# Performance work log

Measured on AMD Instinct MI355X. Metric: run time of the kernel, lower is better.

## Reference

```python
import jax, jax.numpy as jnp
import numpy as np

NEG_SLOPE = 0.2  # PyG GATConv default leaky_relu slope


def gat_conv(x, src, dst, W, a_src, a_dst, b, num_nodes):
    """One PyG-style GATConv layer (concat over heads).
    x: [N, F_in]; src/dst: [E] (message flows src -> dst);
    W: [F_in, H*C]; a_src/a_dst: [H, C]; b: [H*C].
    """
    H, C = a_src.shape
    h = (x @ W).reshape(num_nodes, H, C)              # [N, H, C]
    alpha_src = jnp.sum(h * a_src, axis=-1)           # [N, H]
    alpha_dst = jnp.sum(h * a_dst, axis=-1)           # [N, H]
    e = jax.nn.leaky_relu(alpha_src[src] + alpha_dst[dst], NEG_SLOPE)  # [E, H]
    # segment softmax over incoming edges of each destination node
    m = jax.ops.segment_max(e, dst, num_segments=num_nodes)            # [N, H]
    ex = jnp.exp(e - m[dst])
    s = jax.ops.segment_sum(ex, dst, num_segments=num_nodes)           # [N, H]
    alpha = ex / (s[dst] + 1e-16)                                      # [E, H]
    msg = h[src] * alpha[:, :, None]                                   # [E, H, C]
    out = jax.ops.segment_sum(msg, dst, num_segments=num_nodes)        # [N, H, C]
    return out.reshape(num_nodes, H * C) + b


def setup_inputs() -> dict:
    key = jax.random.key(0)
    ks = jax.random.split(key, 12)
    N, E, F_in, C, H = 50000, 800000, 256, 64, 8
    x = jax.random.normal(ks[0], (N, F_in), dtype=jnp.float32)
    edge_index = jax.random.randint(ks[1], (2, E), 0, N, dtype=jnp.int64)
    glorot = lambda k, shape: jax.random.normal(k, shape, jnp.float32) * np.sqrt(2.0 / (shape[0] + shape[-1]))
    return {
        "x": x,
        "edge_index": edge_index,
        "W1": glorot(ks[2], (F_in, H * C)),
        "att_src1": glorot(ks[3], (H, C)),
        "att_dst1": glorot(ks[4], (H, C)),
        "b1": jnp.zeros((H * C,), jnp.float32),
        "W2": glorot(ks[5], (H * C, 1 * C)),
        "att_src2": glorot(ks[6], (1, C)),
        "att_dst2": glorot(ks[7], (1, C)),
        "b2": jnp.zeros((C,), jnp.float32),
    }


def reference(x, edge_index, W1, att_src1, att_dst1, b1, W2, att_src2, att_dst2, b2):
    N = x.shape[0]
    # add self-loops (PyG GATConv default add_self_loops=True)
    loops = jnp.arange(N, dtype=edge_index.dtype)
    src = jnp.concatenate([edge_index[0], loops])
    dst = jnp.concatenate([edge_index[1], loops])
    h = gat_conv(x, src, dst, W1, att_src1, att_dst1, b1, N)   # [N, 512]
    h = jax.nn.relu(h)                                         # dropout p=0 -> identity
    out = gat_conv(h, src, dst, W2, att_src2, att_dst2, b2, N) # [N, 64]
    return out
```

## Files before the change

kernel.cpp:

```cpp
#include <hip/hip_runtime.h>
#include <hip/hip_bf16.h>
#include <math.h>
#include <type_traits>

#define NEG_SLOPE 0.2f
#define CAP 64

typedef float f32x4 __attribute__((ext_vector_type(4)));
typedef short s16x8 __attribute__((ext_vector_type(8)));
typedef short s16x4 __attribute__((ext_vector_type(4)));

__device__ __forceinline__ float bf2f(ushort s) {
    union { unsigned u; float f; } cv; cv.u = ((unsigned)s) << 16;
    return cv.f;
}
__device__ __forceinline__ ushort f2bf(float f) {
    __hip_bfloat16 b = __float2bfloat16(f);
    union { __hip_bfloat16 b; ushort u; } cv; cv.b = b;
    return cv.u;
}

__device__ __forceinline__ int edge_val(const int* e, long long i, int is64) {
    return is64 ? e[(size_t)(2 * i)] : e[(size_t)i];
}

__global__ __launch_bounds__(256) void prep_k(
        const float* __restrict__ W1, ushort* __restrict__ W1t, int K1, int N1,
        const float* __restrict__ W2, ushort* __restrict__ W2t, int K2, int N2,
        int* __restrict__ counts, int N, int nbW1, int nbW2) {
    int b = blockIdx.x, tid = threadIdx.x;
    if (b < nbW1) {
        int idx = b * 256 + tid;
        if (idx < K1 * N1) {
            int k = idx & (K1 - 1), n = idx / K1;
            W1t[(size_t)n * K1 + k] = f2bf(W1[(size_t)k * N1 + n]);
        }
        return;
    }
    b -= nbW1;
    if (b < nbW2) {
        int idx = b * 256 + tid;
        if (idx < K2 * N2) {
            int k = idx & (K2 - 1), n = idx / K2;
            W2t[(size_t)n * K2 + k] = f2bf(W2[(size_t)k * N2 + n]);
        }
        return;
    }
    b -= nbW2;
    int i = b * 256 + tid;
    if (i < N) counts[i] = 0;
}

template <typename AT, int KK, int NCOLS, int H, int HB>
__device__ __forceinline__ void gemm_bres_core(
        int bx, int by, const AT* __restrict__ A, const ushort* __restrict__ Bt,
        ushort* __restrict__ C,
        const float* __restrict__ att_s, const float* __restrict__ att_d,
        float* __restrict__ as_, float* __restrict__ ad_, int M, int Ntot) {
    constexpr int NT = NCOLS / 16;
    __shared__ __align__(16) ushort Bs[NCOLS][KK + 8];

    int tid = threadIdx.x;
    int wid = tid >> 6, lane = tid & 63;
    int l15 = lane & 15, l4 = lane >> 4;
    int bn = bx * NCOLS;

#pragma unroll
    for (int p = 0; p < NCOLS * KK / (8 * 512); ++p) {
        int idx = p * 512 + tid;
        int n = idx / (KK / 8);
        int kc = (idx % (KK / 8)) << 3;
        *(s16x8*)&Bs[n][kc] = *(const s16x8*)&Bt[(size_t)(bn + n) * KK + kc];
    }

    int mbase = by * 128 + wid * 16;
    int rowA = mbase + l15; if (rowA >= M) rowA = M - 1;
    s16x8 af[KK / 32];
    if constexpr (std::is_same_v<AT, float>) {
        const float* Ap = A + (size_t)rowA * KK + (l4 << 3);
#pragma unroll
        for (int ks = 0; ks < KK / 32; ++ks) {
            float4 u0 = *(const float4*)&Ap[ks * 32];
            float4 u1 = *(const float4*)&Ap[ks * 32 + 4];
            s16x8 w;
            w[0] = (short)f2bf(u0.x); w[1] = (short)f2bf(u0.y);
            w[2] = (short)f2bf(u0.z); w[3] = (short)f2bf(u0.w);
            w[4] = (short)f2bf(u1.x); w[5] = (short)f2bf(u1.y);
            w[6] = (short)f2bf(u1.z); w[7] = (short)f2bf(u1.w);
            af[ks] = w;
        }
    } else {
        const ushort* Ap = A + (size_t)rowA * KK + (l4 << 3);
#pragma unroll
        for (int ks = 0; ks < KK / 32; ++ks) af[ks] = *(const s16x8*)&Ap[ks * 32];
    }

    __syncthreads();

    f32x4 acc[NT] = {};
#pragma unroll
    for (int nt = 0; nt < NT; ++nt) {
#pragma unroll
        for (int ks = 0; ks < KK / 32; ++ks) {
            s16x8 bfr = *(const s16x8*)&Bs[nt * 16 + l15][ks * 32 + (l4 << 3)];
            acc[nt] = __builtin_amdgcn_mfma_f32_16x16x32_bf16(af[ks], bfr, acc[nt], 0, 0, 0);
        }
    }

#pragma unroll
    for (int h = 0; h < HB; ++h) {
        int head = bx * HB + h;
        float asv[4], adv[4];
#pragma unroll
        for (int t = 0; t < 4; ++t) {
            asv[t] = att_s[head * 64 + t * 16 + l15];
            adv[t] = att_d[head * 64 + t * 16 + l15];
        }
#pragma unroll
        for (int j = 0; j < 4; ++j) {
            int r = mbase + (l4 << 2) + j;
            float ps = 0.f, pd = 0.f;
#pragma unroll
            for (int t = 0; t < 4; ++t) {
                float v = acc[h * 4 + t][j];
                ps += v * asv[t];
                pd += v * adv[t];
            }
#pragma unroll
            for (int off = 1; off < 16; off <<= 1) {
                ps += __shfl_xor(ps, off);
                pd += __shfl_xor(pd, off);
            }
            if (r < M) {
                if (l15 == 0) {
                    as_[(size_t)r * H + head] = ps;
                    ad_[(size_t)r * H + head] = pd;
                }
#pragma unroll
                for (int t = 0; t < 4; ++t)
                    C[(size_t)r * Ntot + head * 64 + t * 16 + l15] = f2bf(acc[h * 4 + t][j]);
            }
        }
    }
}

__global__ __launch_bounds__(512) void gemm1_scatter(
        const float* __restrict__ A, const ushort* __restrict__ Bt,
        ushort* __restrict__ C, const float* __restrict__ att_s,
        const float* __restrict__ att_d, float* __restrict__ as_,
        float* __restrict__ ad_, int M, int Ntot, int nby, int nGemm,
        const int* __restrict__ ebuf, int E, int Nn,
        int* __restrict__ counts, int* __restrict__ csr) {
    int g = blockIdx.x;
    if (g < nGemm) {
        int by = (g & 7) + ((g >> 4) << 3);
        int bx = (g >> 3) & 1;
        if (by < nby)
            gemm_bres_core<float, 256, 256, 8, 4>(bx, by, A, Bt, C,
                                                  att_s, att_d, as_, ad_, M, Ntot);
        return;
    }
    __shared__ int s_is64;
    if (threadIdx.x < 64) {
        int v = ebuf[2 * threadIdx.x + 1];
        unsigned long long bl = __ballot(v != 0);
        if (threadIdx.x == 0) s_is64 = (bl == 0ull) ? 1 : 0;
    }
    __syncthreads();
    int is64 = s_is64;
    int i = (g - nGemm) * 512 + threadIdx.x;
    if (i >= E + Nn) return;
    int s, d;
    if (i < E) {
        s = edge_val(ebuf, i, is64);
        d = edge_val(ebuf, (long long)E + i, is64);
    } else {
        s = i - E; d = s;
    }
    int pos = atomicAdd(&counts[d], 1);
    if (pos < CAP) csr[(size_t)d * CAP + pos] = s;
}

template <typename AT, int KK, int NCOLS, int H, int HB>
__global__ __launch_bounds__(512) void gemm_bres(
        const AT* __restrict__ A, const ushort* __restrict__ Bt, ushort* __restrict__ C,
        const float* __restrict__ att_s, const float* __restrict__ att_d,
        float* __restrict__ as_, float* __restrict__ ad_, int M, int Ntot) {
    gemm_bres_core<AT, KK, NCOLS, H, HB>(blockIdx.x, blockIdx.y, A, Bt, C,
                                         att_s, att_d, as_, ad_, M, Ntot);
}

__global__ __launch_bounds__(256) void gat_fused_l1(
        const ushort* __restrict__ h, const float* __restrict__ as_,
        const float* __restrict__ ad_, const int* __restrict__ counts,
        const int* __restrict__ csr, const float* __restrict__ bias,
        ushort* __restrict__ out1, int N) {
    int n = (blockIdx.x * 256 + threadIdx.x) >> 6;
    if (n >= N) return;
    int l = threadIdx.x & 63;
    size_t base = (size_t)n * CAP;
    int deg = counts[n]; deg = deg > CAP ? CAP : deg;

    int hh = l & 7, e0 = l >> 3;
    float adw = ad_[n * 8 + hh];
    float m = -1e30f, s = 0.f;
    for (int k = e0; k < deg; k += 8) {
        int src = csr[base + k];
        float e = as_[src * 8 + hh] + adw;
        e = e > 0.f ? e : NEG_SLOPE * e;
        float mn = fmaxf(m, e);
        s = s * __expf(m - mn) + __expf(e - mn);
        m = mn;
    }
#pragma unroll
    for (int off = 8; off < 64; off <<= 1) {
        float mo = __shfl_xor(m, off), so = __shfl_xor(s, off);
        float mn = fmaxf(m, mo);
        s = s * __expf(m - mn) + so * __expf(mo - mn);
        m = mn;
    }
    float inv = 1.f / (s + 1e-16f);
    int hd = l >> 3;
    float mh   = __shfl(m, hd);
    float invh = __shfl(inv, hd);
    float adh  = __shfl(adw, hd);

    float acc[8] = {};
    int k = 0;
    for (; k + 4 <= deg; k += 4) {
        int s0 = csr[base + k],     s1 = csr[base + k + 1];
        int s2 = csr[base + k + 2], s3 = csr[base + k + 3];
        s16x8 v0 = *(const s16x8*)&h[((size_t)s0 << 9) + (l << 3)];
        s16x8 v1 = *(const s16x8*)&h[((size_t)s1 << 9) + (l << 3)];
        s16x8 v2 = *(const s16x8*)&h[((size_t)s2 << 9) + (l << 3)];
        s16x8 v3 = *(const s16x8*)&h[((size_t)s3 << 9) + (l << 3)];
        float e0v = as_[s0 * 8 + hd] + adh;
        float e1v = as_[s1 * 8 + hd] + adh;
        float e2v = as_[s2 * 8 + hd] + adh;
        float e3v = as_[s3 * 8 + hd] + adh;
        e0v = e0v > 0.f ? e0v : NEG_SLOPE * e0v;
        e1v = e1v > 0.f ? e1v : NEG_SLOPE * e1v;
        e2v = e2v > 0.f ? e2v : NEG_SLOPE * e2v;
        e3v = e3v > 0.f ? e3v : NEG_SLOPE * e3v;
        float a0 = __expf(e0v - mh);
        float a1 = __expf(e1v - mh);
        float a2 = __expf(e2v - mh);
        float a3 = __expf(e3v - mh);
#pragma unroll
        for (int j = 0; j < 8; ++j)
            acc[j] += a0 * bf2f((ushort)v0[j]) + a1 * bf2f((ushort)v1[j])
                    + a2 * bf2f((ushort)v2[j]) + a3 * bf2f((ushort)v3[j]);
    }
    for (; k < deg; ++k) {
        int s0 = csr[base + k];
        s16x8 v0 = *(const s16x8*)&h[((size_t)s0 << 9) + (l << 3)];
        float e0v = as_[s0 * 8 + hd] + adh;
        e0v = e0v > 0.f ? e0v : NEG_SLOPE * e0v;
        float a0 = __expf(e0v - mh);
#pragma unroll
        for (int j = 0; j < 8; ++j) acc[j] += a0 * bf2f((ushort)v0[j]);
    }
    float4 b0 = *(const float4*)&bias[l * 8];
    float4 b1 = *(const float4*)&bias[l * 8 + 4];
    s16x8 w;
    w[0] = f2bf(fmaxf(acc[0] * invh + b0.x, 0.f));
    w[1] = f2bf(fmaxf(acc[1] * invh + b0.y, 0.f));
    w[2] = f2bf(fmaxf(acc[2] * invh + b0.z, 0.f));
    w[3] = f2bf(fmaxf(acc[3] * invh + b0.w, 0.f));
    w[4] = f2bf(fmaxf(acc[4] * invh + b1.x, 0.f));
    w[5] = f2bf(fmaxf(acc[5] * invh + b1.y, 0.f));
    w[6] = f2bf(fmaxf(acc[6] * invh + b1.z, 0.f));
    w[7] = f2bf(fmaxf(acc[7] * invh + b1.w, 0.f));
    *(s16x8*)&out1[((size_t)n << 9) + (l << 3)] = w;
}

__global__ __launch_bounds__(256) void gat_fused_l2(
        const ushort* __restrict__ h, const float* __restrict__ as_,
        const float* __restrict__ ad_, const int* __restrict__ counts,
        const int* __restrict__ csr, const float* __restrict__ bias,
        float* __restrict__ out, int N) {
    int n = (blockIdx.x * 256 + threadIdx.x) >> 6;
    if (n >= N) return;
    int l = threadIdx.x & 63;
    size_t base = (size_t)n * CAP;
    int deg = counts[n]; deg = deg > CAP ? CAP : deg;
    float adv = ad_[n];

    float m = -1e30f, s = 0.f;
    for (int k = l; k < deg; k += 64) {
        float e = as_[csr[base + k]] + adv;
        e = e > 0.f ? e : NEG_SLOPE * e;
        float mn = fmaxf(m, e);
        s = s * __expf(m - mn) + __expf(e - mn);
        m = mn;
    }
#pragma unroll
    for (int off = 1; off < 64; off <<= 1) {
        float mo = __shfl_xor(m, off), so = __shfl_xor(s, off);
        float mn = fmaxf(m, mo);
        s = s * __expf(m - mn) + so * __expf(mo - mn);
        m = mn;
    }
    float inv = 1.f / (s + 1e-16f);

    int q = l >> 4, c4 = l & 15;
    float a0 = 0.f, a1 = 0.f, a2 = 0.f, a3 = 0.f;
    int k = q;
    for (; k + 12 < deg; k += 16) {
        int sA = csr[base + k],     sB = csr[base + k + 4];
        int sC = csr[base + k + 8], sD = csr[base + k + 12];
        s16x4 vA = *(const s16x4*)&h[((size_t)sA << 6) + (c4 << 2)];
        s16x4 vB = *(const s16x4*)&h[((size_t)sB << 6) + (c4 << 2)];
        s16x4 vC = *(const s16x4*)&h[((size_t)sC << 6) + (c4 << 2)];
        s16x4 vD = *(const s16x4*)&h[((size_t)sD << 6) + (c4 << 2)];
        float eA = as_[sA] + adv, eB = as_[sB] + adv;
        float eC = as_[sC] + adv, eD = as_[sD] + adv;
        eA = eA > 0.f ? eA : NEG_SLOPE * eA;
        eB = eB > 0.f ? eB : NEG_SLOPE * eB;
        eC = eC > 0.f ? eC : NEG_SLOPE * eC;
        eD = eD > 0.f ? eD : NEG_SLOPE * eD;
        float aA = __expf(eA - m), aB = __expf(eB - m);
        float aC = __expf(eC - m), aD = __expf(eD - m);
        a0 += aA * bf2f((ushort)vA[0]) + aB * bf2f((ushort)vB[0])
            + aC * bf2f((ushort)vC[0]) + aD * bf2f((ushort)vD[0]);
        a1 += aA * bf2f((ushort)vA[1]) + aB * bf2f((ushort)vB[1])
            + aC * bf2f((ushort)vC[1]) + aD * bf2f((ushort)vD[1]);
        a2 += aA * bf2f((ushort)vA[2]) + aB * bf2f((ushort)vB[2])
            + aC * bf2f((ushort)vC[2]) + aD * bf2f((ushort)vD[2]);
        a3 += aA * bf2f((ushort)vA[3]) + aB * bf2f((ushort)vB[3])
            + aC * bf2f((ushort)vC[3]) + aD * bf2f((ushort)vD[3]);
    }
    for (; k < deg; k += 4) {
        int sA = csr[base + k];
        s16x4 vA = *(const s16x4*)&h[((size_t)sA << 6) + (c4 << 2)];
        float eA = as_[sA] + adv;
        eA = eA > 0.f ? eA : NEG_SLOPE * eA;
        float aA = __expf(eA - m);
        a0 += aA * bf2f((ushort)vA[0]);
        a1 += aA * bf2f((ushort)vA[1]);
        a2 += aA * bf2f((ushort)vA[2]);
        a3 += aA * bf2f((ushort)vA[3]);
    }
    a0 += __shfl_xor(a0, 16); a0 += __shfl_xor(a0, 32);
    a1 += __shfl_xor(a1, 16); a1 += __shfl_xor(a1, 32);
    a2 += __shfl_xor(a2, 16); a2 += __shfl_xor(a2, 32);
    a3 += __shfl_xor(a3, 16); a3 += __shfl_xor(a3, 32);
    if (q == 0) {
        float4 bv = *(const float4*)&bias[c4 << 2];
        float4 r;
        r.x = a0 * inv + bv.x; r.y = a1 * inv + bv.y;
        r.z = a2 * inv + bv.z; r.w = a3 * inv + bv.w;
        *(float4*)&out[((size_t)n << 6) + (c4 << 2)] = r;
    }
}

extern "C" void kernel_launch(void* const* d_in, const int* in_sizes, int n_in,
                              void* d_out, int out_size, void* d_ws, size_t ws_size,
                              hipStream_t stream) {
    const float* x    = (const float*)d_in[0];
    const int*   ebuf = (const int*)d_in[1];
    const float* W1   = (const float*)d_in[2];
    const float* aS1  = (const float*)d_in[3];
    const float* aD1  = (const float*)d_in[4];
    const float* b1   = (const float*)d_in[5];
    const float* W2   = (const float*)d_in[6];
    const float* aS2  = (const float*)d_in[7];
    const float* aD2  = (const float*)d_in[8];
    const float* b2   = (const float*)d_in[9];
    float* out = (float*)d_out;

    const int F_in = 256, H1 = 8, HC1 = 512, C2 = 64;
    int N = in_sizes[0] / F_in;
    int E = in_sizes[1] / 2;

    char* ws = (char*)d_ws;
    size_t off = 0;
    auto alloc = [&](size_t bytes) -> void* {
        void* p = ws + off;
        off = (off + bytes + 255) & ~(size_t)255;
        return p;
    };
    ushort* h1b    = (ushort*)alloc((size_t)N * HC1 * 2);
    ushort* out1b  = (ushort*)alloc((size_t)N * HC1 * 2);
    float* as1     = (float*)alloc((size_t)N * H1 * 4);
    float* ad1     = (float*)alloc((size_t)N * H1 * 4);
    float* as2     = (float*)alloc((size_t)N * 4);
    float* ad2     = (float*)alloc((size_t)N * 4);
    int*   counts  = (int*)alloc((size_t)N * 4);
    int*   csr     = (int*)alloc((size_t)N * CAP * 4);
    ushort* W1t    = (ushort*)alloc((size_t)F_in * HC1 * 2);
    ushort* W2t    = (ushort*)alloc((size_t)HC1 * C2 * 2);
    ushort* h2b    = h1b;

    int nbW1 = (F_in * HC1 + 255) >> 8;
    int nbW2 = (HC1 * C2 + 255) >> 8;
    int nbZ  = (N + 255) >> 8;

    prep_k<<<nbW1 + nbW2 + nbZ, 256, 0, stream>>>(
        W1, W1t, F_in, HC1, W2, W2t, HC1, C2, counts, N, nbW1, nbW2);

    {
        int nby = (N + 127) / 128;
        int nbyPad = (nby + 7) & ~7;
        int nGemm = 2 * nbyPad;
        int nScatter = (E + N + 511) / 512;
        gemm1_scatter<<<nGemm + nScatter, 512, 0, stream>>>(
            x, W1t, h1b, aS1, aD1, as1, ad1, N, HC1, nby, nGemm,
            ebuf, E, N, counts, csr);
    }

    gat_fused_l1<<<(N + 3) / 4, 256, 0, stream>>>(h1b, as1, ad1, counts, csr, b1, out1b, N);

    {
        dim3 g(1, (N + 127) / 128);
        gemm_bres<ushort, 512, 64, 1, 1><<<g, 512, 0, stream>>>(
            out1b, W2t, h2b, aS2, aD2, as2, ad2, N, C2);
    }

    gat_fused_l2<<<(N + 3) / 4, 256, 0, stream>>>(h2b, as2, ad2, counts, csr, b2, out, N);
}
```

Measured before the change: 288.0 us.

## Fuse layer-2 GEMM and attention projections into layer-1 aggregation kernel

The layer-1 aggregation kernel now multiplies each node's 512-wide relu output by W2 directly, using scalar FMAs and wave shuffles, and writes a 64-wide bf16 h2. This removes the 50000x512 intermediate write and re-read and one kernel launch. The layer-2 attention scalars are computed from precomputed W2·att vectors built in the prep kernel, computed from the fp32 W2 rather than from rounded h2. The layer-1 GEMM now has each block cover all 512 columns in two passes, so the A tile is loaded and converted once. The cost is heavy per-lane scalar math and shuffle reductions in the gather kernel in place of MFMA.

```diff
diff --git a/kernel.cpp b/kernel.cpp
--- a/kernel.cpp
+++ b/kernel.cpp
@@ -27,6 +27,8 @@
 __global__ __launch_bounds__(256) void prep_k(
         const float* __restrict__ W1, ushort* __restrict__ W1t, int K1, int N1,
         const float* __restrict__ W2, ushort* __restrict__ W2t, int K2, int N2,
+        const float* __restrict__ aS2, const float* __restrict__ aD2,
+        float* __restrict__ w2s, float* __restrict__ w2d,
         int* __restrict__ counts, int N, int nbW1, int nbW2) {
     int b = blockIdx.x, tid = threadIdx.x;
     if (b < nbW1) {
@@ -47,117 +49,113 @@
         return;
     }
     b -= nbW2;
+    if (b < 2) {
+        int k = b * 256 + tid;
+        if (k < K2) {
+            float s = 0.f, d = 0.f;
+            for (int c = 0; c < N2; ++c) {
+                float w = W2[(size_t)k * N2 + c];
+                s += w * aS2[c];
+                d += w * aD2[c];
+            }
+            w2s[k] = s; w2d[k] = d;
+        }
+        return;
+    }
+    b -= 2;
     int i = b * 256 + tid;
     if (i < N) counts[i] = 0;
-}
-
-template <typename AT, int KK, int NCOLS, int H, int HB>
-__device__ __forceinline__ void gemm_bres_core(
-        int bx, int by, const AT* __restrict__ A, const ushort* __restrict__ Bt,
-        ushort* __restrict__ C,
-        const float* __restrict__ att_s, const float* __restrict__ att_d,
-        float* __restrict__ as_, float* __restrict__ ad_, int M, int Ntot) {
-    constexpr int NT = NCOLS / 16;
-    __shared__ __align__(16) ushort Bs[NCOLS][KK + 8];
-
-    int tid = threadIdx.x;
-    int wid = tid >> 6, lane = tid & 63;
-    int l15 = lane & 15, l4 = lane >> 4;
-    int bn = bx * NCOLS;
-
-#pragma unroll
-    for (int p = 0; p < NCOLS * KK / (8 * 512); ++p) {
-        int idx = p * 512 + tid;
-        int n = idx / (KK / 8);
-        int kc = (idx % (KK / 8)) << 3;
-        *(s16x8*)&Bs[n][kc] = *(const s16x8*)&Bt[(size_t)(bn + n) * KK + kc];
-    }
-
-    int mbase = by * 128 + wid * 16;
-    int rowA = mbase + l15; if (rowA >= M) rowA = M - 1;
-    s16x8 af[KK / 32];
-    if constexpr (std::is_same_v<AT, float>) {
-        const float* Ap = A + (size_t)rowA * KK + (l4 << 3);
-#pragma unroll
-        for (int ks = 0; ks < KK / 32; ++ks) {
-            float4 u0 = *(const float4*)&Ap[ks * 32];
-            float4 u1 = *(const float4*)&Ap[ks * 32 + 4];
-            s16x8 w;
-            w[0] = (short)f2bf(u0.x); w[1] = (short)f2bf(u0.y);
-            w[2] = (short)f2bf(u0.z); w[3] = (short)f2bf(u0.w);
-            w[4] = (short)f2bf(u1.x); w[5] = (short)f2bf(u1.y);
-            w[6] = (short)f2bf(u1.z); w[7] = (short)f2bf(u1.w);
-            af[ks] = w;
-        }
-    } else {
-        const ushort* Ap = A + (size_t)rowA * KK + (l4 << 3);
-#pragma unroll
-        for (int ks = 0; ks < KK / 32; ++ks) af[ks] = *(const s16x8*)&Ap[ks * 32];
-    }
-
-    __syncthreads();
-
-    f32x4 acc[NT] = {};
-#pragma unroll
-    for (int nt = 0; nt < NT; ++nt) {
-#pragma unroll
-        for (int ks = 0; ks < KK / 32; ++ks) {
-            s16x8 bfr = *(const s16x8*)&Bs[nt * 16 + l15][ks * 32 + (l4 << 3)];
-            acc[nt] = __builtin_amdgcn_mfma_f32_16x16x32_bf16(af[ks], bfr, acc[nt], 0, 0, 0);
-        }
-    }
-
-#pragma unroll
-    for (int h = 0; h < HB; ++h) {
-        int head = bx * HB + h;
-        float asv[4], adv[4];
-#pragma unroll
-        for (int t = 0; t < 4; ++t) {
-            asv[t] = att_s[head * 64 + t * 16 + l15];
-            adv[t] = att_d[head * 64 + t * 16 + l15];
-        }
-#pragma unroll
-        for (int j = 0; j < 4; ++j) {
-            int r = mbase + (l4 << 2) + j;
-            float ps = 0.f, pd = 0.f;
-#pragma unroll
-            for (int t = 0; t < 4; ++t) {
-                float v = acc[h * 4 + t][j];
-                ps += v * asv[t];
-                pd += v * adv[t];
-            }
-#pragma unroll
-            for (int off = 1; off < 16; off <<= 1) {
-                ps += __shfl_xor(ps, off);
-                pd += __shfl_xor(pd, off);
-            }
-            if (r < M) {
-                if (l15 == 0) {
-                    as_[(size_t)r * H + head] = ps;
-                    ad_[(size_t)r * H + head] = pd;
-                }
-#pragma unroll
-                for (int t = 0; t < 4; ++t)
-                    C[(size_t)r * Ntot + head * 64 + t * 16 + l15] = f2bf(acc[h * 4 + t][j]);
-            }
-        }
-    }
 }
 
 __global__ __launch_bounds__(512) void gemm1_scatter(
         const float* __restrict__ A, const ushort* __restrict__ Bt,
         ushort* __restrict__ C, const float* __restrict__ att_s,
         const float* __restrict__ att_d, float* __restrict__ as_,
-        float* __restrict__ ad_, int M, int Ntot, int nby, int nGemm,
+        float* __restrict__ ad_, int M, int Ntot, int nGemm,
         const int* __restrict__ ebuf, int E, int Nn,
         int* __restrict__ counts, int* __restrict__ csr) {
     int g = blockIdx.x;
     if (g < nGemm) {
-        int by = (g & 7) + ((g >> 4) << 3);
-        int bx = (g >> 3) & 1;
-        if (by < nby)
-            gemm_bres_core<float, 256, 256, 8, 4>(bx, by, A, Bt, C,
-                                                  att_s, att_d, as_, ad_, M, Ntot);
+        constexpr int KK = 256, NCOLS = 256, NT = 16;
+        __shared__ __align__(16) ushort Bs[NCOLS][KK + 8];
+        int tid = threadIdx.x;
+        int wid = tid >> 6, lane = tid & 63;
+        int l15 = lane & 15, l4 = lane >> 4;
+        int mbase = g * 128 + wid * 16;
+        int rowA = mbase + l15; if (rowA >= M) rowA = M - 1;
+
+        s16x8 af[8];
+        {
+            const float* Ap = A + (size_t)rowA * KK + (l4 << 3);
+#pragma unroll
+            for (int ks = 0; ks < 8; ++ks) {
+                float4 u0 = *(const float4*)&Ap[ks * 32];
+                float4 u1 = *(const float4*)&Ap[ks * 32 + 4];
+                s16x8 w;
+                w[0] = (short)f2bf(u0.x); w[1] = (short)f2bf(u0.y);
+                w[2] = (short)f2bf(u0.z); w[3] = (short)f2bf(u0.w);
+                w[4] = (short)f2bf(u1.x); w[5] = (short)f2bf(u1.y);
+                w[6] = (short)f2bf(u1.z); w[7] = (short)f2bf(u1.w);
+                af[ks] = w;
+            }
+        }
+
+#pragma unroll
+        for (int px = 0; px < 2; ++px) {
+            int bn = px * NCOLS;
+#pragma unroll
+            for (int p = 0; p < 16; ++p) {
+                int idx = p * 512 + tid;
+                int n = idx >> 5;
+                int kc = (idx & 31) << 3;
+                *(s16x8*)&Bs[n][kc] = *(const s16x8*)&Bt[(size_t)(bn + n) * KK + kc];
+            }
+            __syncthreads();
+            f32x4 acc[NT] = {};
+#pragma unroll
+            for (int nt = 0; nt < NT; ++nt)
+#pragma unroll
+                for (int ks = 0; ks < 8; ++ks) {
+                    s16x8 bfr = *(const s16x8*)&Bs[nt * 16 + l15][ks * 32 + (l4 << 3)];
+                    acc[nt] = __builtin_amdgcn_mfma_f32_16x16x32_bf16(af[ks], bfr, acc[nt], 0, 0, 0);
+                }
+            __syncthreads();
+#pragma unroll
+            for (int h = 0; h < 4; ++h) {
+                int head = px * 4 + h;
+                float asv[4], adv[4];
+#pragma unroll
+                for (int t = 0; t < 4; ++t) {
+                    asv[t] = att_s[head * 64 + t * 16 + l15];
+                    adv[t] = att_d[head * 64 + t * 16 + l15];
+                }
+#pragma unroll
+                for (int j = 0; j < 4; ++j) {
+                    int r = mbase + (l4 << 2) + j;
+                    float ps = 0.f, pd = 0.f;
+#pragma unroll
+                    for (int t = 0; t < 4; ++t) {
+                        float v = acc[h * 4 + t][j];
+                        ps += v * asv[t];
+                        pd += v * adv[t];
+                    }
+#pragma unroll
+                    for (int off = 1; off < 16; off <<= 1) {
+                        ps += __shfl_xor(ps, off);
+                        pd += __shfl_xor(pd, off);
+                    }
+                    if (r < M) {
+                        if (l15 == 0) {
+                            as_[(size_t)r * 8 + head] = ps;
+                            ad_[(size_t)r * 8 + head] = pd;
+                        }
+#pragma unroll
+                        for (int t = 0; t < 4; ++t)
+                            C[(size_t)r * Ntot + head * 64 + t * 16 + l15] = f2bf(acc[h * 4 + t][j]);
+                    }
+                }
+            }
+        }
         return;
     }
     __shared__ int s_is64;
@@ -181,20 +179,13 @@
     if (pos < CAP) csr[(size_t)d * CAP + pos] = s;
 }
 
-template <typename AT, int KK, int NCOLS, int H, int HB>
-__global__ __launch_bounds__(512) void gemm_bres(
-        const AT* __restrict__ A, const ushort* __restrict__ Bt, ushort* __restrict__ C,
-        const float* __restrict__ att_s, const float* __restrict__ att_d,
-        float* __restrict__ as_, float* __restrict__ ad_, int M, int Ntot) {
-    gemm_bres_core<AT, KK, NCOLS, H, HB>(blockIdx.x, blockIdx.y, A, Bt, C,
-                                         att_s, att_d, as_, ad_, M, Ntot);
-}
-
 __global__ __launch_bounds__(256) void gat_fused_l1(
         const ushort* __restrict__ h, const float* __restrict__ as_,
         const float* __restrict__ ad_, const int* __restrict__ counts,
         const int* __restrict__ csr, const float* __restrict__ bias,
-        ushort* __restrict__ out1, int N) {
+        const ushort* __restrict__ W2t, const float* __restrict__ w2s,
+        const float* __restrict__ w2d, ushort* __restrict__ h2,
+        float* __restrict__ as2, float* __restrict__ ad2, int N) {
     int n = (blockIdx.x * 256 + threadIdx.x) >> 6;
     if (n >= N) return;
     int l = threadIdx.x & 63;
@@ -260,18 +251,63 @@
 #pragma unroll
         for (int j = 0; j < 8; ++j) acc[j] += a0 * bf2f((ushort)v0[j]);
     }
+
     float4 b0 = *(const float4*)&bias[l * 8];
     float4 b1 = *(const float4*)&bias[l * 8 + 4];
-    s16x8 w;
-    w[0] = f2bf(fmaxf(acc[0] * invh + b0.x, 0.f));
-    w[1] = f2bf(fmaxf(acc[1] * invh + b0.y, 0.f));
-    w[2] = f2bf(fmaxf(acc[2] * invh + b0.z, 0.f));
-    w[3] = f2bf(fmaxf(acc[3] * invh + b0.w, 0.f));
-    w[4] = f2bf(fmaxf(acc[4] * invh + b1.x, 0.f));
-    w[5] = f2bf(fmaxf(acc[5] * invh + b1.y, 0.f));
-    w[6] = f2bf(fmaxf(acc[6] * invh + b1.z, 0.f));
-    w[7] = f2bf(fmaxf(acc[7] * invh + b1.w, 0.f));
-    *(s16x8*)&out1[((size_t)n << 9) + (l << 3)] = w;
+    float rr[8];
+    rr[0] = fmaxf(acc[0] * invh + b0.x, 0.f);
+    rr[1] = fmaxf(acc[1] * invh + b0.y, 0.f);
+    rr[2] = fmaxf(acc[2] * invh + b0.z, 0.f);
+    rr[3] = fmaxf(acc[3] * invh + b0.w, 0.f);
+    rr[4] = fmaxf(acc[4] * invh + b1.x, 0.f);
+    rr[5] = fmaxf(acc[5] * invh + b1.y, 0.f);
+    rr[6] = fmaxf(acc[6] * invh + b1.z, 0.f);
+    rr[7] = fmaxf(acc[7] * invh + b1.w, 0.f);
+
+    {
+        float4 wsa = *(const float4*)&w2s[l << 3];
+        float4 wsb = *(const float4*)&w2s[(l << 3) + 4];
+        float4 wda = *(const float4*)&w2d[l << 3];
+        float4 wdb = *(const float4*)&w2d[(l << 3) + 4];
+        float ps = rr[0] * wsa.x + rr[1] * wsa.y + rr[2] * wsa.z + rr[3] * wsa.w
+                 + rr[4] * wsb.x + rr[5] * wsb.y + rr[6] * wsb.z + rr[7] * wsb.w;
+        float pd = rr[0] * wda.x + rr[1] * wda.y + rr[2] * wda.z + rr[3] * wda.w
+                 + rr[4] * wdb.x + rr[5] * wdb.y + rr[6] * wdb.z + rr[7] * wdb.w;
+#pragma unroll
+        for (int off = 1; off < 64; off <<= 1) {
+            ps += __shfl_xor(ps, off);
+            pd += __shfl_xor(pd, off);
+        }
+        if (l == 0) { as2[n] = ps; ad2[n] = pd; }
+    }
+
+#pragma unroll
+    for (int cc = 0; cc < 16; ++cc) {
+        int c0 = cc * 4;
+        s16x8 q0 = *(const s16x8*)&W2t[(size_t)(c0 + 0) * 512 + (l << 3)];
+        s16x8 q1 = *(const s16x8*)&W2t[(size_t)(c0 + 1) * 512 + (l << 3)];
+        s16x8 q2 = *(const s16x8*)&W2t[(size_t)(c0 + 2) * 512 + (l << 3)];
+        s16x8 q3 = *(const s16x8*)&W2t[(size_t)(c0 + 3) * 512 + (l << 3)];
+        float p0 = 0.f, p1 = 0.f, p2 = 0.f, p3 = 0.f;
+#pragma unroll
+        for (int j = 0; j < 8; ++j) {
+            p0 += rr[j] * bf2f((ushort)q0[j]);
+            p1 += rr[j] * bf2f((ushort)q1[j]);
+            p2 += rr[j] * bf2f((ushort)q2[j]);
+            p3 += rr[j] * bf2f((ushort)q3[j]);
+        }
+        float t0 = __shfl_xor(p0, 1), t2 = __shfl_xor(p2, 1);
+        float t1 = __shfl_xor(p1, 1), t3 = __shfl_xor(p3, 1);
+        float u0 = (l & 1) ? p2 + t2 : p0 + t0;
+        float u1 = (l & 1) ? p3 + t3 : p1 + t1;
+        float s0 = __shfl_xor(u0, 2), s1 = __shfl_xor(u1, 2);
+        float v = (l & 2) ? u1 + s1 : u0 + s0;
+        v += __shfl_xor(v, 4);
+        v += __shfl_xor(v, 8);
+        v += __shfl_xor(v, 16);
+        v += __shfl_xor(v, 32);
+        if (l < 4) h2[((size_t)n << 6) + c0 + ((l & 1) << 1) + ((l >> 1) & 1)] = f2bf(v);
+    }
 }
 
 __global__ __launch_bounds__(256) void gat_fused_l2(
@@ -381,7 +417,7 @@
         return p;
     };
     ushort* h1b    = (ushort*)alloc((size_t)N * HC1 * 2);
-    ushort* out1b  = (ushort*)alloc((size_t)N * HC1 * 2);
+    ushort* h2b    = (ushort*)alloc((size_t)N * C2 * 2);
     float* as1     = (float*)alloc((size_t)N * H1 * 4);
     float* ad1     = (float*)alloc((size_t)N * H1 * 4);
     float* as2     = (float*)alloc((size_t)N * 4);
@@ -390,32 +426,27 @@
     int*   csr     = (int*)alloc((size_t)N * CAP * 4);
     ushort* W1t    = (ushort*)alloc((size_t)F_in * HC1 * 2);
     ushort* W2t    = (ushort*)alloc((size_t)HC1 * C2 * 2);
-    ushort* h2b    = h1b;
+    float* w2s     = (float*)alloc((size_t)HC1 * 4);
+    float* w2d     = (float*)alloc((size_t)HC1 * 4);
 
     int nbW1 = (F_in * HC1 + 255) >> 8;
     int nbW2 = (HC1 * C2 + 255) >> 8;
     int nbZ  = (N + 255) >> 8;
 
-    prep_k<<<nbW1 + nbW2 + nbZ, 256, 0, stream>>>(
-        W1, W1t, F_in, HC1, W2, W2t, HC1, C2, counts, N, nbW1, nbW2);
+    prep_k<<<nbW1 + nbW2 + 2 + nbZ, 256, 0, stream>>>(
+        W1, W1t, F_in, HC1, W2, W2t, HC1, C2, aS2, aD2, w2s, w2d,
+        counts, N, nbW1, nbW2);
 
     {
-        int nby = (N + 127) / 128;
-        int nbyPad = (nby + 7) & ~7;
-        int nGemm = 2 * nbyPad;
+        int nGemm = (N + 127) / 128;
         int nScatter = (E + N + 511) / 512;
         gemm1_scatter<<<nGemm + nScatter, 512, 0, stream>>>(
-            x, W1t, h1b, aS1, aD1, as1, ad1, N, HC1, nby, nGemm,
+            x, W1t, h1b, aS1, aD1, as1, ad1, N, HC1, nGemm,
             ebuf, E, N, counts, csr);
     }
 
-    gat_fused_l1<<<(N + 3) / 4, 256, 0, stream>>>(h1b, as1, ad1, counts, csr, b1, out1b, N);
-
-    {
-        dim3 g(1, (N + 127) / 128);
-        gemm_bres<ushort, 512, 64, 1, 1><<<g, 512, 0, stream>>>(
-            out1b, W2t, h2b, aS2, aD2, as2, ad2, N, C2);
-    }
+    gat_fused_l1<<<(N + 3) / 4, 256, 0, stream>>>(
+        h1b, as1, ad1, counts, csr, b1, W2t, w2s, w2d, h2b, as2, ad2, N);
 
     gat_fused_l2<<<(N + 3) / 4, 256, 0, stream>>>(h2b, as2, ad2, counts, csr, b2, out, N);
 }
```

Result: slower. 332.5 us (+15.5%).

## Load each A row tile once and loop over all output column chunks in GEMM1

Applied to the files above, without the earlier changes.

GEMM1 previously split the 512 output columns across two blocks, so each block re-read and re-converted the same fp32 A rows. Now one block per 128-row tile converts its A fragments once and loops over four 128-column chunks of W1, reloading B into shared memory each time. This halves A traffic and the fp32-to-bf16 conversion work. In exchange it adds barriers per chunk, serialises the B loads within a block, and launches fewer GEMM blocks. GEMM2 is specialised into a dedicated non-template kernel with the same behaviour.

```diff
diff --git a/kernel.cpp b/kernel.cpp
--- a/kernel.cpp
+++ b/kernel.cpp
@@ -51,113 +51,95 @@
     if (i < N) counts[i] = 0;
 }
 
-template <typename AT, int KK, int NCOLS, int H, int HB>
-__device__ __forceinline__ void gemm_bres_core(
-        int bx, int by, const AT* __restrict__ A, const ushort* __restrict__ Bt,
-        ushort* __restrict__ C,
-        const float* __restrict__ att_s, const float* __restrict__ att_d,
-        float* __restrict__ as_, float* __restrict__ ad_, int M, int Ntot) {
-    constexpr int NT = NCOLS / 16;
-    __shared__ __align__(16) ushort Bs[NCOLS][KK + 8];
-
-    int tid = threadIdx.x;
-    int wid = tid >> 6, lane = tid & 63;
-    int l15 = lane & 15, l4 = lane >> 4;
-    int bn = bx * NCOLS;
-
-#pragma unroll
-    for (int p = 0; p < NCOLS * KK / (8 * 512); ++p) {
-        int idx = p * 512 + tid;
-        int n = idx / (KK / 8);
-        int kc = (idx % (KK / 8)) << 3;
-        *(s16x8*)&Bs[n][kc] = *(const s16x8*)&Bt[(size_t)(bn + n) * KK + kc];
-    }
-
-    int mbase = by * 128 + wid * 16;
-    int rowA = mbase + l15; if (rowA >= M) rowA = M - 1;
-    s16x8 af[KK / 32];
-    if constexpr (std::is_same_v<AT, float>) {
-        const float* Ap = A + (size_t)rowA * KK + (l4 << 3);
-#pragma unroll
-        for (int ks = 0; ks < KK / 32; ++ks) {
-            float4 u0 = *(const float4*)&Ap[ks * 32];
-            float4 u1 = *(const float4*)&Ap[ks * 32 + 4];
-            s16x8 w;
-            w[0] = (short)f2bf(u0.x); w[1] = (short)f2bf(u0.y);
-            w[2] = (short)f2bf(u0.z); w[3] = (short)f2bf(u0.w);
-            w[4] = (short)f2bf(u1.x); w[5] = (short)f2bf(u1.y);
-            w[6] = (short)f2bf(u1.z); w[7] = (short)f2bf(u1.w);
-            af[ks] = w;
-        }
-    } else {
-        const ushort* Ap = A + (size_t)rowA * KK + (l4 << 3);
-#pragma unroll
-        for (int ks = 0; ks < KK / 32; ++ks) af[ks] = *(const s16x8*)&Ap[ks * 32];
-    }
-
-    __syncthreads();
-
-    f32x4 acc[NT] = {};
-#pragma unroll
-    for (int nt = 0; nt < NT; ++nt) {
-#pragma unroll
-        for (int ks = 0; ks < KK / 32; ++ks) {
-            s16x8 bfr = *(const s16x8*)&Bs[nt * 16 + l15][ks * 32 + (l4 << 3)];
-            acc[nt] = __builtin_amdgcn_mfma_f32_16x16x32_bf16(af[ks], bfr, acc[nt], 0, 0, 0);
-        }
-    }
-
-#pragma unroll
-    for (int h = 0; h < HB; ++h) {
-        int head = bx * HB + h;
-        float asv[4], adv[4];
-#pragma unroll
-        for (int t = 0; t < 4; ++t) {
-            asv[t] = att_s[head * 64 + t * 16 + l15];
-            adv[t] = att_d[head * 64 + t * 16 + l15];
-        }
-#pragma unroll
-        for (int j = 0; j < 4; ++j) {
-            int r = mbase + (l4 << 2) + j;
-            float ps = 0.f, pd = 0.f;
-#pragma unroll
-            for (int t = 0; t < 4; ++t) {
-                float v = acc[h * 4 + t][j];
-                ps += v * asv[t];
-                pd += v * adv[t];
-            }
-#pragma unroll
-            for (int off = 1; off < 16; off <<= 1) {
-                ps += __shfl_xor(ps, off);
-                pd += __shfl_xor(pd, off);
-            }
-            if (r < M) {
-                if (l15 == 0) {
-                    as_[(size_t)r * H + head] = ps;
-                    ad_[(size_t)r * H + head] = pd;
-                }
-#pragma unroll
-                for (int t = 0; t < 4; ++t)
-                    C[(size_t)r * Ntot + head * 64 + t * 16 + l15] = f2bf(acc[h * 4 + t][j]);
-            }
-        }
-    }
-}
-
 __global__ __launch_bounds__(512) void gemm1_scatter(
         const float* __restrict__ A, const ushort* __restrict__ Bt,
         ushort* __restrict__ C, const float* __restrict__ att_s,
         const float* __restrict__ att_d, float* __restrict__ as_,
-        float* __restrict__ ad_, int M, int Ntot, int nby, int nGemm,
+        float* __restrict__ ad_, int M, int Ntot, int nGemm,
         const int* __restrict__ ebuf, int E, int Nn,
         int* __restrict__ counts, int* __restrict__ csr) {
     int g = blockIdx.x;
     if (g < nGemm) {
-        int by = (g & 7) + ((g >> 4) << 3);
-        int bx = (g >> 3) & 1;
-        if (by < nby)
-            gemm_bres_core<float, 256, 256, 8, 4>(bx, by, A, Bt, C,
-                                                  att_s, att_d, as_, ad_, M, Ntot);
+        constexpr int KK = 256, NCOLS = 128, NT = 8;
+        __shared__ __align__(16) ushort Bs[NCOLS][KK + 8];
+        int tid = threadIdx.x;
+        int wid = tid >> 6, lane = tid & 63;
+        int l15 = lane & 15, l4 = lane >> 4;
+        int mbase = g * 128 + wid * 16;
+        int rowA = mbase + l15; if (rowA >= M) rowA = M - 1;
+
+        s16x8 af[8];
+        {
+            const float* Ap = A + (size_t)rowA * KK + (l4 << 3);
+#pragma unroll
+            for (int ks = 0; ks < 8; ++ks) {
+                float4 u0 = *(const float4*)&Ap[ks * 32];
+                float4 u1 = *(const float4*)&Ap[ks * 32 + 4];
+                s16x8 w;
+                w[0] = (short)f2bf(u0.x); w[1] = (short)f2bf(u0.y);
+                w[2] = (short)f2bf(u0.z); w[3] = (short)f2bf(u0.w);
+                w[4] = (short)f2bf(u1.x); w[5] = (short)f2bf(u1.y);
+                w[6] = (short)f2bf(u1.z); w[7] = (short)f2bf(u1.w);
+                af[ks] = w;
+            }
+        }
+
+#pragma unroll
+        for (int px = 0; px < 4; ++px) {
+            int bn = px * NCOLS;
+            if (px) __syncthreads();
+#pragma unroll
+            for (int p = 0; p < 8; ++p) {
+                int idx = p * 512 + tid;
+                int n = idx >> 5;
+                int kc = (idx & 31) << 3;
+                *(s16x8*)&Bs[n][kc] = *(const s16x8*)&Bt[(size_t)(bn + n) * KK + kc];
+            }
+            __syncthreads();
+            f32x4 acc[NT] = {};
+#pragma unroll
+            for (int nt = 0; nt < NT; ++nt)
+#pragma unroll
+                for (int ks = 0; ks < 8; ++ks) {
+                    s16x8 bfr = *(const s16x8*)&Bs[nt * 16 + l15][ks * 32 + (l4 << 3)];
+                    acc[nt] = __builtin_amdgcn_mfma_f32_16x16x32_bf16(af[ks], bfr, acc[nt], 0, 0, 0);
+                }
+#pragma unroll
+            for (int h = 0; h < 2; ++h) {
+                int head = px * 2 + h;
+                float asv[4], adv[4];
+#pragma unroll
+                for (int t = 0; t < 4; ++t) {
+                    asv[t] = att_s[head * 64 + t * 16 + l15];
+                    adv[t] = att_d[head * 64 + t * 16 + l15];
+                }
+#pragma unroll
+                for (int j = 0; j < 4; ++j) {
+                    int r = mbase + (l4 << 2) + j;
+                    float ps = 0.f, pd = 0.f;
+#pragma unroll
+                    for (int t = 0; t < 4; ++t) {
+                        float v = acc[h * 4 + t][j];
+                        ps += v * asv[t];
+                        pd += v * adv[t];
+                    }
+#pragma unroll
+                    for (int off = 1; off < 16; off <<= 1) {
+                        ps += __shfl_xor(ps, off);
+                        pd += __shfl_xor(pd, off);
+                    }
+                    if (r < M) {
+                        if (l15 == 0) {
+                            as_[(size_t)r * 8 + head] = ps;
+                            ad_[(size_t)r * 8 + head] = pd;
+                        }
+#pragma unroll
+                        for (int t = 0; t < 4; ++t)
+                            C[(size_t)r * Ntot + head * 64 + t * 16 + l15] = f2bf(acc[h * 4 + t][j]);
+                    }
+                }
+            }
+        }
         return;
     }
     __shared__ int s_is64;
@@ -181,13 +163,70 @@
     if (pos < CAP) csr[(size_t)d * CAP + pos] = s;
 }
 
-template <typename AT, int KK, int NCOLS, int H, int HB>
-__global__ __launch_bounds__(512) void gemm_bres(
-        const AT* __restrict__ A, const ushort* __restrict__ Bt, ushort* __restrict__ C,
+__global__ __launch_bounds__(512) void gemm2_bres(
+        const ushort* __restrict__ A, const ushort* __restrict__ Bt, ushort* __restrict__ C,
         const float* __restrict__ att_s, const float* __restrict__ att_d,
-        float* __restrict__ as_, float* __restrict__ ad_, int M, int Ntot) {
-    gemm_bres_core<AT, KK, NCOLS, H, HB>(blockIdx.x, blockIdx.y, A, Bt, C,
-                                         att_s, att_d, as_, ad_, M, Ntot);
+        float* __restrict__ as_, float* __restrict__ ad_, int M) {
+    constexpr int KK = 512, NCOLS = 64, NT = 4;
+    __shared__ __align__(16) ushort Bs[NCOLS][KK + 8];
+    int tid = threadIdx.x;
+    int wid = tid >> 6, lane = tid & 63;
+    int l15 = lane & 15, l4 = lane >> 4;
+
+#pragma unroll
+    for (int p = 0; p < NCOLS * KK / (8 * 512); ++p) {
+        int idx = p * 512 + tid;
+        int n = idx >> 6;
+        int kc = (idx & 63) << 3;
+        *(s16x8*)&Bs[n][kc] = *(const s16x8*)&Bt[(size_t)n * KK + kc];
+    }
+
+    int mbase = blockIdx.y * 128 + wid * 16;
+    int rowA = mbase + l15; if (rowA >= M) rowA = M - 1;
+    const ushort* Ap = A + (size_t)rowA * KK + (l4 << 3);
+    s16x8 af[16];
+#pragma unroll
+    for (int ks = 0; ks < 16; ++ks) af[ks] = *(const s16x8*)&Ap[ks * 32];
+
+    __syncthreads();
+
+    f32x4 acc[NT] = {};
+#pragma unroll
+    for (int nt = 0; nt < NT; ++nt)
+#pragma unroll
+        for (int ks = 0; ks < 16; ++ks) {
+            s16x8 bfr = *(const s16x8*)&Bs[nt * 16 + l15][ks * 32 + (l4 << 3)];
+            acc[nt] = __builtin_amdgcn_mfma_f32_16x16x32_bf16(af[ks], bfr, acc[nt], 0, 0, 0);
+        }
+
+    float asv[NT], adv[NT];
+#pragma unroll
+    for (int t = 0; t < NT; ++t) {
+        asv[t] = att_s[t * 16 + l15];
+        adv[t] = att_d[t * 16 + l15];
+    }
+#pragma unroll
+    for (int j = 0; j < 4; ++j) {
+        int r = mbase + (l4 << 2) + j;
+        float ps = 0.f, pd = 0.f;
+#pragma unroll
+        for (int t = 0; t < NT; ++t) {
+            float v = acc[t][j];
+            ps += v * asv[t];
+            pd += v * adv[t];
+        }
+#pragma unroll
+        for (int off = 1; off < 16; off <<= 1) {
+            ps += __shfl_xor(ps, off);
+            pd += __shfl_xor(pd, off);
+        }
+        if (r < M) {
+            if (l15 == 0) { as_[r] = ps; ad_[r] = pd; }
+#pragma unroll
+            for (int t = 0; t < NT; ++t)
+                C[((size_t)r << 6) + t * 16 + l15] = f2bf(acc[t][j]);
+        }
+    }
 }
 
 __global__ __launch_bounds__(256) void gat_fused_l1(
@@ -400,12 +439,10 @@
         W1, W1t, F_in, HC1, W2, W2t, HC1, C2, counts, N, nbW1, nbW2);
 
     {
-        int nby = (N + 127) / 128;
-        int nbyPad = (nby + 7) & ~7;
-        int nGemm = 2 * nbyPad;
+        int nGemm = (N + 127) / 128;
         int nScatter = (E + N + 511) / 512;
         gemm1_scatter<<<nGemm + nScatter, 512, 0, stream>>>(
-            x, W1t, h1b, aS1, aD1, as1, ad1, N, HC1, nby, nGemm,
+            x, W1t, h1b, aS1, aD1, as1, ad1, N, HC1, nGemm,
             ebuf, E, N, counts, csr);
     }
 
@@ -413,8 +450,7 @@
 
     {
         dim3 g(1, (N + 127) / 128);
-        gemm_bres<ushort, 512, 64, 1, 1><<<g, 512, 0, stream>>>(
-            out1b, W2t, h2b, aS2, aD2, as2, ad2, N, C2);
+        gemm2_bres<<<g, 512, 0, stream>>>(out1b, W2t, h2b, aS2, aD2, as2, ad2, N);
     }
 
     gat_fused_l2<<<(N + 3) / 4, 256, 0, stream>>>(h2b, as2, ad2, counts, csr, b2, out, N);
```

Result: faster. 260.7 us (-9.5%).
